# Kernel optimization log

Hardware: AMD Instinct MI355X
Metric: run time of the kernel (lower is better)

Reference implementation:

```python
import jax, jax.numpy as jnp
import numpy as np

B, S, D, H = 4, 2048, 512, 8
DH = D // H


def setup_inputs() -> dict:
    key = jax.random.key(0)
    ks = jax.random.split(key, 6)
    embeddings = jax.random.normal(ks[0], (B, S, D), dtype=jnp.float32)
    token_masks = jax.random.randint(ks[1], (B, S), 0, 2, dtype=jnp.int32)
    # keras 'random_normal' initializer: stddev 0.05
    Wq = 0.05 * jax.random.normal(ks[2], (D, D), dtype=jnp.float32)
    Wk = 0.05 * jax.random.normal(ks[3], (D, D), dtype=jnp.float32)
    Wv = 0.05 * jax.random.normal(ks[4], (D, D), dtype=jnp.float32)
    Wo = 0.05 * jax.random.normal(ks[5], (D, D), dtype=jnp.float32)
    return {"embeddings": embeddings, "token_masks": token_masks,
            "Wq": Wq, "Wk": Wk, "Wv": Wv, "Wo": Wo}


def reference(embeddings, token_masks, Wq, Wk, Wv, Wo):
    b, s, d = embeddings.shape
    h, dh = H, d // H
    # QKV projections -> (b, h, s, dh)
    def split_heads(x):
        return x.reshape(b, s, h, dh).transpose(0, 2, 1, 3)
    Q = split_heads(embeddings @ Wq)
    K = split_heads(embeddings @ Wk)
    V = split_heads(embeddings @ Wv)
    scores = jnp.einsum('bhqd,bhkd->bhqk', Q, K) / jnp.sqrt(jnp.float32(dh))
    # causal (lower-triangular) mask combined with padding mask on both q and k
    causal = jnp.tril(jnp.ones((s, s), dtype=jnp.float32))
    tm = token_masks.astype(jnp.float32)
    attn_mask = causal[None, None, :, :] * tm[:, None, None, :] * tm[:, None, :, None]
    scores = jnp.where(attn_mask > 0, scores, jnp.float32(-1e30))
    weights = jax.nn.softmax(scores, axis=-1)  # dropout omitted (inference/eval mode)
    context = jnp.einsum('bhqk,bhkd->bhqd', weights, V)
    context = context.transpose(0, 2, 1, 3).reshape(b, s, d)
    return context @ Wo
```

## Files before the change

### kernel.cpp

```cpp
#include <hip/hip_runtime.h>
#include <hip/hip_bf16.h>
#include <stdint.h>

#define BATCH 4
#define SEQ 2048
#define DMODEL 512
#define NHEAD 8
#define HD 64

#define C1 0.18033688f
#define BIAS2 -23.0831207f

using f32x4 = __attribute__((ext_vector_type(4))) float;
using bfrag = __attribute__((ext_vector_type(8))) short;

__device__ __forceinline__ short f2bf(float f) {
  uint32_t x = __builtin_bit_cast(uint32_t, f);
  uint32_t r = (x + 0x7fffu + ((x >> 16) & 1u)) >> 16;
  return (short)r;
}
__device__ __forceinline__ short f2bf_fast(float f) {
  return (short)((__builtin_bit_cast(uint32_t, f) + 0x8000u) >> 16);
}
__device__ __forceinline__ float bf2f(short s) {
  return __builtin_bit_cast(float, ((uint32_t)(uint16_t)s) << 16);
}
__device__ __forceinline__ void gl_lds16(const void* g, void* l) {
  __builtin_amdgcn_global_load_lds(
      (const __attribute__((address_space(1))) void*)g,
      (__attribute__((address_space(3))) void*)l, 16, 0, 0);
}
__device__ __forceinline__ bool sniff_f32(const void* p, int tid) {
  const uint32_t* xw = (const uint32_t*)p;
  const int lane = tid & 63;
  const uint32_t w1 = xw[lane], w2 = xw[64 + lane];
  bool bad = (((w1 >> 7) & 0xffu) >= 0xB0u) | (((w1 >> 23) & 0xffu) >= 0xB0u) |
             (((w2 >> 7) & 0xffu) >= 0xB0u) | (((w2 >> 23) & 0xffu) >= 0xB0u);
  return __ballot(bad) != 0ull;
}

__global__ __launch_bounds__(256) void conv_x(const void* __restrict__ in,
                                              short* __restrict__ out) {
  const int tid = threadIdx.x;
  const bool isf32 = sniff_f32(in, tid);
  const int i = (blockIdx.x * 256 + tid) * 8;
  if (isf32) {
    const float* f = (const float*)in;
    short r[8];
#pragma unroll
    for (int j = 0; j < 8; ++j) r[j] = f2bf(f[i + j]);
    *(bfrag*)&out[i] = *(bfrag*)r;
  } else {
    *(bfrag*)&out[i] = *(const bfrag*)&((const short*)in)[i];
  }
}

__global__ __launch_bounds__(256) void transpose_w4(const void* __restrict__ w0,
                                                    const void* __restrict__ w1,
                                                    const void* __restrict__ w2,
                                                    const void* __restrict__ w3,
                                                    short* __restrict__ outAll) {
  __shared__ short t[32][33];
  const int z = blockIdx.z;
  const void* in = (z == 0) ? w0 : (z == 1) ? w1 : (z == 2) ? w2 : w3;
  short* out = outAll + (size_t)z * DMODEL * DMODEL;
  const int tx = threadIdx.x, ty = threadIdx.y;
  const int tid = ty * 32 + tx;
  const bool isf32 = sniff_f32(in, tid);
  const int n0 = blockIdx.x * 32, k0 = blockIdx.y * 32;
#pragma unroll
  for (int i = ty; i < 32; i += 8) {
    const int idx = (k0 + i) * DMODEL + n0 + tx;
    t[i][tx] = isf32 ? f2bf(((const float*)in)[idx]) : ((const short*)in)[idx];
  }
  __syncthreads();
#pragma unroll
  for (int i = ty; i < 32; i += 8) out[(n0 + i) * DMODEL + k0 + tx] = t[tx][i];
}

__global__ __launch_bounds__(256) void gemm_qkv(const short* __restrict__ X,
                                                const short* __restrict__ WtAll,
                                                short* __restrict__ Qo,
                                                short* __restrict__ Ko,
                                                short* __restrict__ Vo) {
  __shared__ __align__(16) short As[128 * 32];
  __shared__ __align__(16) short Bs[128 * 32];
  const int which = blockIdx.z;
  const short* Wt = WtAll + which * DMODEL * DMODEL;
  const int m0 = blockIdx.y * 128, n0 = blockIdx.x * 128;
  const int tid = threadIdx.x, lane = tid & 63, wave = tid >> 6;
  const int l15 = lane & 15, quad = lane >> 4;
  const int wm = wave >> 1, wn = wave & 1;
  const int lrow = lane >> 2, lcol = (lane & 3) * 8;
  f32x4 acc[4][4] = {};
  for (int kc = 0; kc < DMODEL; kc += 32) {
#pragma unroll
    for (int i = 0; i < 2; ++i) {
      const int r0 = (wave * 2 + i) * 16;
      gl_lds16(&X[(size_t)(m0 + r0 + lrow) * DMODEL + kc + lcol], &As[r0 * 32]);
      gl_lds16(&Wt[(size_t)(n0 + r0 + lrow) * DMODEL + kc + lcol], &Bs[r0 * 32]);
    }
    __syncthreads();
    bfrag a[4], b[4];
#pragma unroll
    for (int t = 0; t < 4; ++t) {
      a[t] = *(const bfrag*)&As[(wm * 64 + t * 16 + l15) * 32 + quad * 8];
      b[t] = *(const bfrag*)&Bs[(wn * 64 + t * 16 + l15) * 32 + quad * 8];
    }
#pragma unroll
    for (int tm = 0; tm < 4; ++tm)
#pragma unroll
      for (int tn = 0; tn < 4; ++tn)
        acc[tm][tn] = __builtin_amdgcn_mfma_f32_16x16x32_bf16(a[tm], b[tn], acc[tm][tn], 0, 0, 0);
    __syncthreads();
  }
  short* O = (which == 0) ? Qo : (which == 1) ? Ko : Vo;
#pragma unroll
  for (int tn = 0; tn < 4; ++tn) {
    const int col = n0 + wn * 64 + tn * 16 + l15;
    const int h = col >> 6, d = col & 63;
#pragma unroll
    for (int tm = 0; tm < 4; ++tm) {
#pragma unroll
      for (int r = 0; r < 4; ++r) {
        const int row = m0 + wm * 64 + tm * 16 + quad * 4 + r;
        const int b = row >> 11, s = row & 2047;
        O[((b * NHEAD + h) * SEQ + s) * HD + d] = f2bf(acc[tm][tn][r]);
      }
    }
  }
}

__global__ __launch_bounds__(256) void gemm_out(const short* __restrict__ X,
                                                const short* __restrict__ Wt,
                                                float* __restrict__ O) {
  __shared__ __align__(16) short As[128 * 32];
  __shared__ __align__(16) short Bs[128 * 32];
  const int m0 = blockIdx.y * 128, n0 = blockIdx.x * 128;
  const int tid = threadIdx.x, lane = tid & 63, wave = tid >> 6;
  const int l15 = lane & 15, quad = lane >> 4;
  const int wm = wave >> 1, wn = wave & 1;
  const int lrow = lane >> 2, lcol = (lane & 3) * 8;
  f32x4 acc[4][4] = {};
  for (int kc = 0; kc < DMODEL; kc += 32) {
#pragma unroll
    for (int i = 0; i < 2; ++i) {
      const int r0 = (wave * 2 + i) * 16;
      gl_lds16(&X[(size_t)(m0 + r0 + lrow) * DMODEL + kc + lcol], &As[r0 * 32]);
      gl_lds16(&Wt[(size_t)(n0 + r0 + lrow) * DMODEL + kc + lcol], &Bs[r0 * 32]);
    }
    __syncthreads();
    bfrag a[4], b[4];
#pragma unroll
    for (int t = 0; t < 4; ++t) {
      a[t] = *(const bfrag*)&As[(wm * 64 + t * 16 + l15) * 32 + quad * 8];
      b[t] = *(const bfrag*)&Bs[(wn * 64 + t * 16 + l15) * 32 + quad * 8];
    }
#pragma unroll
    for (int tm = 0; tm < 4; ++tm)
#pragma unroll
      for (int tn = 0; tn < 4; ++tn)
        acc[tm][tn] = __builtin_amdgcn_mfma_f32_16x16x32_bf16(a[tm], b[tn], acc[tm][tn], 0, 0, 0);
    __syncthreads();
  }
#pragma unroll
  for (int tm = 0; tm < 4; ++tm)
#pragma unroll
    for (int tn = 0; tn < 4; ++tn) {
      const int col = n0 + wn * 64 + tn * 16 + l15;
#pragma unroll
      for (int r = 0; r < 4; ++r) {
        const int row = m0 + wm * 64 + tm * 16 + quad * 4 + r;
        O[(size_t)row * DMODEL + col] = acc[tm][tn][r];
      }
    }
}

__global__ __launch_bounds__(256) void meanv(const short* __restrict__ V,
                                             float* __restrict__ mv) {
  __shared__ float red[32][64];
  const int bh = blockIdx.x >> 3, seg = blockIdx.x & 7;
  const int tid = threadIdx.x, sg = tid & 7, kk = tid >> 3;
  const size_t base = (size_t)bh * SEQ * HD;
  float acc[8] = {};
  for (int k = seg * 256 + kk; k < seg * 256 + 256; k += 32) {
    bfrag v = *(const bfrag*)&V[base + (size_t)k * HD + sg * 8];
#pragma unroll
    for (int j = 0; j < 8; ++j) acc[j] += bf2f(v[j]);
  }
#pragma unroll
  for (int j = 0; j < 8; ++j) red[kk][sg * 8 + j] = acc[j];
  __syncthreads();
  if (tid < 64) {
    float s = 0.f;
#pragma unroll
    for (int k2 = 0; k2 < 32; ++k2) s += red[k2][tid];
    atomicAdd(&mv[bh * 64 + tid], s * (1.f / 2048.f));
  }
}

__global__ __launch_bounds__(256, 4) void attn(const short* __restrict__ Q,
                                               const short* __restrict__ K,
                                               const short* __restrict__ V,
                                               const int* __restrict__ tmask,
                                               const float* __restrict__ meanV,
                                               short* __restrict__ ctx) {
  __shared__ __align__(16) short Ks[64 * 72];
  __shared__ __align__(16) short Vts[64 * 64];
  __shared__ __align__(16) short Ps[4 * 16 * 64];
  __shared__ int tmq[64];
  __shared__ int tmk[64];
  const int m2 = blockIdx.x >> 3, a3 = blockIdx.x & 7;
  const int j2 = blockIdx.y >> 3, b3 = blockIdx.y & 7;
  const int quart = (m2 + j2) & 3;
  const int qi = quart * 8 + ((quart & 1) ? (7 - a3) : a3);
  const int bh = j2 * 8 + b3;
  const int b = bh >> 3, h = bh & 7;
  const int q0 = qi * 64;
  const int tid = threadIdx.x, lane = tid & 63, wave = tid >> 6;
  const int l15 = lane & 15, quad = lane >> 4;
  const size_t base = (size_t)bh * SEQ * HD;

  bfrag qa0 = *(const bfrag*)&Q[base + (size_t)(q0 + wave * 16 + l15) * HD + quad * 8];
  bfrag qa1 = *(const bfrag*)&Q[base + (size_t)(q0 + wave * 16 + l15) * HD + 32 + quad * 8];
  if (tid < 64) tmq[tid] = tmask[b * SEQ + q0 + tid];

  f32x4 accO[4] = {};
  float lrow[4] = {0.f, 0.f, 0.f, 0.f};

  const int rp = tid >> 3, sgp = tid & 7;
  bfrag kA, kB, vA, vB;
  int tmreg = 0;

  auto prefetch = [&](int kc) {
    const size_t o0 = base + (size_t)(kc + 2 * rp) * HD + sgp * 8;
    kA = *(const bfrag*)&K[o0];
    kB = *(const bfrag*)&K[o0 + HD];
    vA = *(const bfrag*)&V[o0];
    vB = *(const bfrag*)&V[o0 + HD];
    if (tid < 64) tmreg = tmask[b * SEQ + kc + tid];
  };
  auto store_lds = [&]() {
    *(bfrag*)&Ks[(2 * rp) * 72 + sgp * 8] = kA;
    *(bfrag*)&Ks[(2 * rp + 1) * 72 + sgp * 8] = kB;
    const int g = ((rp >> 2) ^ sgp) & 7;
    const int kpos = (2 * rp) & 7;
#pragma unroll
    for (int j = 0; j < 8; ++j) {
      const uint32_t w = (uint32_t)(uint16_t)vA[j] | ((uint32_t)(uint16_t)vB[j] << 16);
      *(uint32_t*)&Vts[(sgp * 8 + j) * 64 + g * 8 + kpos] = w;
    }
    if (tid < 64) tmk[tid] = tmreg;
  };
  auto compute = [&](bool diag) {
    f32x4 sacc[4] = {};
#pragma unroll
    for (int t = 0; t < 4; ++t) {
      bfrag b0 = *(const bfrag*)&Ks[(t * 16 + l15) * 72 + quad * 8];
      sacc[t] = __builtin_amdgcn_mfma_f32_16x16x32_bf16(qa0, b0, sacc[t], 0, 0, 0);
    }
#pragma unroll
    for (int t = 0; t < 4; ++t) {
      bfrag b1 = *(const bfrag*)&Ks[(t * 16 + l15) * 72 + 32 + quad * 8];
      sacc[t] = __builtin_amdgcn_mfma_f32_16x16x32_bf16(qa1, b1, sacc[t], 0, 0, 0);
    }
    float badd[4];
#pragma unroll
    for (int t = 0; t < 4; ++t) badd[t] = tmk[t * 16 + l15] ? BIAS2 : -1e30f;
#pragma unroll
    for (int r = 0; r < 4; ++r) {
      const int m = quad * 4 + r;
#pragma unroll
      for (int t = 0; t < 4; ++t) {
        float p = exp2f(fmaf(sacc[t][r], C1, badd[t]));
        if (diag && (t * 16 + l15 > wave * 16 + m)) p = 0.f;
        lrow[r] += p;
        const int g = ((t * 2 + (l15 >> 3)) ^ (m & 7) ^ ((m >> 3) << 1)) & 7;
        Ps[wave * 1024 + m * 64 + g * 8 + (l15 & 7)] = f2bf_fast(p);
      }
    }
#pragma unroll
    for (int ks = 0; ks < 2; ++ks) {
#pragma unroll
      for (int t = 0; t < 4; ++t) {
        const int gp = ((ks * 4 + quad) ^ (l15 & 7) ^ ((l15 >> 3) << 1)) & 7;
        bfrag pa = *(const bfrag*)&Ps[wave * 1024 + l15 * 64 + gp * 8];
        const int d = t * 16 + l15;
        const int gv = ((ks * 4 + quad) ^ (d >> 3)) & 7;
        bfrag vb = *(const bfrag*)&Vts[d * 64 + gv * 8];
        accO[t] = __builtin_amdgcn_mfma_f32_16x16x32_bf16(pa, vb, accO[t], 0, 0, 0);
      }
    }
  };

  prefetch(0);
  for (int kc = 0; kc < q0; kc += 64) {
    __syncthreads();
    store_lds();
    prefetch(kc + 64);
    __syncthreads();
    compute(false);
  }
  __syncthreads();
  store_lds();
  __syncthreads();
  compute(true);

#pragma unroll
  for (int r = 0; r < 4; ++r) {
    float l = lrow[r];
    l += __shfl_xor(l, 1);
    l += __shfl_xor(l, 2);
    l += __shfl_xor(l, 4);
    l += __shfl_xor(l, 8);
    lrow[r] = 1.f / l;
  }
  const int qrow_loc = wave * 16 + quad * 4;
#pragma unroll
  for (int t = 0; t < 4; ++t) {
    const int d = t * 16 + l15;
    const float mvd = meanV[bh * 64 + d];
#pragma unroll
    for (int r = 0; r < 4; ++r) {
      const int row = qrow_loc + r;
      float val = accO[t][r] * lrow[r];
      if (tmq[row] == 0) val = mvd;
      ctx[((size_t)(b * SEQ + q0 + row)) * DMODEL + h * HD + d] = f2bf(val);
    }
  }
}

extern "C" void kernel_launch(void* const* d_in, const int* in_sizes, int n_in,
                              void* d_out, int out_size, void* d_ws, size_t ws_size,
                              hipStream_t stream) {
  const void* X = d_in[0];
  const int* tmask = (const int*)d_in[1];
  const void* Wq = d_in[2];
  const void* Wk = d_in[3];
  const void* Wv = d_in[4];
  const void* Wo = d_in[5];
  float* out = (float*)d_out;
  char* ws = (char*)d_ws;

  const size_t WELEM = (size_t)DMODEL * DMODEL;
  const size_t TELEM = (size_t)BATCH * NHEAD * SEQ * HD;

  float* mv = (float*)(ws + 4096);
  short* wt = (short*)(ws + 4096 + 8192);
  short* Xb = (short*)(ws + 4096 + 8192 + 2097152);
  short* Qb = Xb + TELEM;
  short* Kb = Qb + TELEM;
  short* Vb = Kb + TELEM;
  short* Cb = Vb + TELEM;

  hipMemsetAsync(mv, 0, 32 * 64 * sizeof(float), stream);
  conv_x<<<(int)(TELEM / (256 * 8)), 256, 0, stream>>>(X, Xb);
  transpose_w4<<<dim3(16, 16, 4), dim3(32, 8), 0, stream>>>(Wq, Wk, Wv, Wo, wt);
  gemm_qkv<<<dim3(4, 64, 3), 256, 0, stream>>>(Xb, wt, Qb, Kb, Vb);
  meanv<<<256, 256, 0, stream>>>(Vb, mv);
  attn<<<dim3(32, 32), 256, 0, stream>>>(Qb, Kb, Vb, tmask, mv, Cb);
  gemm_out<<<dim3(4, 64), 256, 0, stream>>>(Cb, wt + 3 * WELEM, out);
}
```

Before: 187.0 us.

## Merge prep kernels, fuse mean-V into QKV GEMM epilogue, restructure attention loop

Combines the X conversion, weight transposes and mean-V buffer zeroing into one prep launch, which removes the memset and one kernel launch. The mean of V per head is now accumulated from the fp32 GEMM accumulators with atomics in the QKV epilogue, so the separate meanv pass that re-read V is gone. The attention main loop now handles the diagonal tile inside the loop and issues the prefetch after the second barrier. This cuts launches and memory traffic, but adds many atomics in the V GEMM epilogue and changes how prefetch overlaps with compute.

```diff
diff --git a/kernel.cpp b/kernel.cpp
--- a/kernel.cpp
+++ b/kernel.cpp
@@ -39,50 +39,56 @@
   return __ballot(bad) != 0ull;
 }
 
-__global__ __launch_bounds__(256) void conv_x(const void* __restrict__ in,
-                                              short* __restrict__ out) {
-  const int tid = threadIdx.x;
-  const bool isf32 = sniff_f32(in, tid);
-  const int i = (blockIdx.x * 256 + tid) * 8;
-  if (isf32) {
-    const float* f = (const float*)in;
-    short r[8];
-#pragma unroll
-    for (int j = 0; j < 8; ++j) r[j] = f2bf(f[i + j]);
-    *(bfrag*)&out[i] = *(bfrag*)r;
+__global__ __launch_bounds__(256) void prep(const void* __restrict__ X,
+                                            const void* __restrict__ w0,
+                                            const void* __restrict__ w1,
+                                            const void* __restrict__ w2,
+                                            const void* __restrict__ w3,
+                                            short* __restrict__ Xb,
+                                            short* __restrict__ wtAll,
+                                            float* __restrict__ mv) {
+  const int blk = blockIdx.x, tid = threadIdx.x;
+  if (blk < 2048) {
+    const bool isf32 = sniff_f32(X, tid);
+    const int i = (blk * 256 + tid) * 8;
+    if (isf32) {
+      const float* f = (const float*)X;
+      short r[8];
+#pragma unroll
+      for (int j = 0; j < 8; ++j) r[j] = f2bf(f[i + j]);
+      *(bfrag*)&Xb[i] = *(bfrag*)r;
+    } else {
+      *(bfrag*)&Xb[i] = *(const bfrag*)&((const short*)X)[i];
+    }
+  } else if (blk < 3072) {
+    __shared__ short t[32][33];
+    const int idx = blk - 2048;
+    const int z = idx >> 8, rem = idx & 255;
+    const void* in = (z == 0) ? w0 : (z == 1) ? w1 : (z == 2) ? w2 : w3;
+    short* out = wtAll + (size_t)z * DMODEL * DMODEL;
+    const int tx = tid & 31, ty = tid >> 5;
+    const bool isf32 = sniff_f32(in, tid);
+    const int n0 = (rem & 15) * 32, k0 = (rem >> 4) * 32;
+#pragma unroll
+    for (int i = ty; i < 32; i += 8) {
+      const int idx2 = (k0 + i) * DMODEL + n0 + tx;
+      t[i][tx] = isf32 ? f2bf(((const float*)in)[idx2]) : ((const short*)in)[idx2];
+    }
+    __syncthreads();
+#pragma unroll
+    for (int i = ty; i < 32; i += 8) out[(n0 + i) * DMODEL + k0 + tx] = t[tx][i];
   } else {
-    *(bfrag*)&out[i] = *(const bfrag*)&((const short*)in)[i];
-  }
-}
-
-__global__ __launch_bounds__(256) void transpose_w4(const void* __restrict__ w0,
-                                                    const void* __restrict__ w1,
-                                                    const void* __restrict__ w2,
-                                                    const void* __restrict__ w3,
-                                                    short* __restrict__ outAll) {
-  __shared__ short t[32][33];
-  const int z = blockIdx.z;
-  const void* in = (z == 0) ? w0 : (z == 1) ? w1 : (z == 2) ? w2 : w3;
-  short* out = outAll + (size_t)z * DMODEL * DMODEL;
-  const int tx = threadIdx.x, ty = threadIdx.y;
-  const int tid = ty * 32 + tx;
-  const bool isf32 = sniff_f32(in, tid);
-  const int n0 = blockIdx.x * 32, k0 = blockIdx.y * 32;
-#pragma unroll
-  for (int i = ty; i < 32; i += 8) {
-    const int idx = (k0 + i) * DMODEL + n0 + tx;
-    t[i][tx] = isf32 ? f2bf(((const float*)in)[idx]) : ((const short*)in)[idx];
-  }
-  __syncthreads();
-#pragma unroll
-  for (int i = ty; i < 32; i += 8) out[(n0 + i) * DMODEL + k0 + tx] = t[tx][i];
+#pragma unroll
+    for (int j = 0; j < 8; ++j) mv[tid * 8 + j] = 0.f;
+  }
 }
 
 __global__ __launch_bounds__(256) void gemm_qkv(const short* __restrict__ X,
                                                 const short* __restrict__ WtAll,
                                                 short* __restrict__ Qo,
                                                 short* __restrict__ Ko,
-                                                short* __restrict__ Vo) {
+                                                short* __restrict__ Vo,
+                                                float* __restrict__ mv) {
   __shared__ __align__(16) short As[128 * 32];
   __shared__ __align__(16) short Bs[128 * 32];
   const int which = blockIdx.z;
@@ -126,6 +132,24 @@
         const int row = m0 + wm * 64 + tm * 16 + quad * 4 + r;
         const int b = row >> 11, s = row & 2047;
         O[((b * NHEAD + h) * SEQ + s) * HD + d] = f2bf(acc[tm][tn][r]);
+      }
+    }
+  }
+  if (which == 2) {
+    const int b = (m0 + wm * 64) >> 11;
+#pragma unroll
+    for (int tn = 0; tn < 4; ++tn) {
+      float s = 0.f;
+#pragma unroll
+      for (int tm = 0; tm < 4; ++tm)
+#pragma unroll
+        for (int r = 0; r < 4; ++r) s += acc[tm][tn][r];
+      s += __shfl_xor(s, 16);
+      s += __shfl_xor(s, 32);
+      if (quad == 0) {
+        const int col = n0 + wn * 64 + tn * 16 + l15;
+        const int h = col >> 6, d = col & 63;
+        atomicAdd(&mv[(b * NHEAD + h) * 64 + d], s);
       }
     }
   }
@@ -174,29 +198,6 @@
         O[(size_t)row * DMODEL + col] = acc[tm][tn][r];
       }
     }
-}
-
-__global__ __launch_bounds__(256) void meanv(const short* __restrict__ V,
-                                             float* __restrict__ mv) {
-  __shared__ float red[32][64];
-  const int bh = blockIdx.x >> 3, seg = blockIdx.x & 7;
-  const int tid = threadIdx.x, sg = tid & 7, kk = tid >> 3;
-  const size_t base = (size_t)bh * SEQ * HD;
-  float acc[8] = {};
-  for (int k = seg * 256 + kk; k < seg * 256 + 256; k += 32) {
-    bfrag v = *(const bfrag*)&V[base + (size_t)k * HD + sg * 8];
-#pragma unroll
-    for (int j = 0; j < 8; ++j) acc[j] += bf2f(v[j]);
-  }
-#pragma unroll
-  for (int j = 0; j < 8; ++j) red[kk][sg * 8 + j] = acc[j];
-  __syncthreads();
-  if (tid < 64) {
-    float s = 0.f;
-#pragma unroll
-    for (int k2 = 0; k2 < 32; ++k2) s += red[k2][tid];
-    atomicAdd(&mv[bh * 64 + tid], s * (1.f / 2048.f));
-  }
 }
 
 __global__ __launch_bounds__(256, 4) void attn(const short* __restrict__ Q,
@@ -294,17 +295,13 @@
   };
 
   prefetch(0);
-  for (int kc = 0; kc < q0; kc += 64) {
+  for (int kc = 0; kc <= q0; kc += 64) {
     __syncthreads();
     store_lds();
-    prefetch(kc + 64);
-    __syncthreads();
-    compute(false);
-  }
-  __syncthreads();
-  store_lds();
-  __syncthreads();
-  compute(true);
+    __syncthreads();
+    if (kc < q0) prefetch(kc + 64);
+    compute(kc == q0);
+  }
 
 #pragma unroll
   for (int r = 0; r < 4; ++r) {
@@ -319,7 +316,7 @@
 #pragma unroll
   for (int t = 0; t < 4; ++t) {
     const int d = t * 16 + l15;
-    const float mvd = meanV[bh * 64 + d];
+    const float mvd = meanV[bh * 64 + d] * (1.f / 2048.f);
 #pragma unroll
     for (int r = 0; r < 4; ++r) {
       const int row = qrow_loc + r;
@@ -353,11 +350,8 @@
   short* Vb = Kb + TELEM;
   short* Cb = Vb + TELEM;
 
-  hipMemsetAsync(mv, 0, 32 * 64 * sizeof(float), stream);
-  conv_x<<<(int)(TELEM / (256 * 8)), 256, 0, stream>>>(X, Xb);
-  transpose_w4<<<dim3(16, 16, 4), dim3(32, 8), 0, stream>>>(Wq, Wk, Wv, Wo, wt);
-  gemm_qkv<<<dim3(4, 64, 3), 256, 0, stream>>>(Xb, wt, Qb, Kb, Vb);
-  meanv<<<256, 256, 0, stream>>>(Vb, mv);
+  prep<<<3073, 256, 0, stream>>>(X, Wq, Wk, Wv, Wo, Xb, wt, mv);
+  gemm_qkv<<<dim3(4, 64, 3), 256, 0, stream>>>(Xb, wt, Qb, Kb, Vb, mv);
   attn<<<dim3(32, 32), 256, 0, stream>>>(Qb, Kb, Vb, tmask, mv, Cb);
   gemm_out<<<dim3(4, 64), 256, 0, stream>>>(Cb, wt + 3 * WELEM, out);
 }
```

New measurement: 180.7 us. 3.4% less time.
